# Optimization experiments

Hardware: AMD Instinct MI355X
Metric: run time of the kernel (lower is better)

Reference implementation:

```python
import jax, jax.numpy as jnp
import numpy as np

EPS = 1e-5

def _ln(x, g, b):
    m = jnp.mean(x, -1, keepdims=True)
    v = jnp.mean((x - m) ** 2, -1, keepdims=True)
    return (x - m) * jax.lax.rsqrt(v + EPS) * g + b

def _lstm(x, Wih, Whh, bih, bhh):
    # x: [B, T, D]; torch gate order i, f, g, o; h0 = c0 = 0
    B = x.shape[0]
    H = Whh.shape[1]
    h0 = jnp.zeros((B, H), x.dtype)
    c0 = jnp.zeros((B, H), x.dtype)
    bias = bih + bhh
    def step(carry, xt):
        h, c = carry
        gates = xt @ Wih.T + h @ Whh.T + bias  # [B, 4H]
        i, f, g, o = jnp.split(gates, 4, axis=-1)
        c = jax.nn.sigmoid(f) * c + jax.nn.sigmoid(i) * jnp.tanh(g)
        h = jax.nn.sigmoid(o) * jnp.tanh(c)
        return (h, c), h
    _, hs = jax.lax.scan(step, (h0, c0), jnp.swapaxes(x, 0, 1))
    return jnp.swapaxes(hs, 0, 1)  # [B, T, H]

def setup_inputs() -> dict:
    key = jax.random.key(0)
    ks = jax.random.split(key, 20)
    N, C, F, T = 4, 64, 256, 256
    D, H = 128, 32  # LSTM in/out
    s = 0.05
    inp = {
        "inputs": jax.random.normal(ks[0], (N, C, F, T, 2), jnp.float32),
        "ln1_g": jnp.ones((D,), jnp.float32), "ln1_b": jnp.zeros((D,), jnp.float32),
        "Wih_q": s * jax.random.normal(ks[1], (4 * H, D), jnp.float32),
        "Whh_q": s * jax.random.normal(ks[2], (4 * H, H), jnp.float32),
        "bih_q": s * jax.random.normal(ks[3], (4 * H,), jnp.float32),
        "bhh_q": s * jax.random.normal(ks[4], (4 * H,), jnp.float32),
        "Wih_k": s * jax.random.normal(ks[5], (4 * H, D), jnp.float32),
        "Whh_k": s * jax.random.normal(ks[6], (4 * H, H), jnp.float32),
        "bih_k": s * jax.random.normal(ks[7], (4 * H,), jnp.float32),
        "bhh_k": s * jax.random.normal(ks[8], (4 * H,), jnp.float32),
        "Wih_v": s * jax.random.normal(ks[9], (4 * H, D), jnp.float32),
        "Whh_v": s * jax.random.normal(ks[10], (4 * H, H), jnp.float32),
        "bih_v": s * jax.random.normal(ks[11], (4 * H,), jnp.float32),
        "bhh_v": s * jax.random.normal(ks[12], (4 * H,), jnp.float32),
        "ln2_g": jnp.ones((H,), jnp.float32), "ln2_b": jnp.zeros((H,), jnp.float32),
        "Wr": s * jax.random.normal(ks[13], (C, H // 2), jnp.float32),
        "br": s * jax.random.normal(ks[14], (C,), jnp.float32),
        "Wi": s * jax.random.normal(ks[15], (C, H // 2), jnp.float32),
        "bi": s * jax.random.normal(ks[16], (C,), jnp.float32),
        "ln3_g": jnp.ones((C,), jnp.float32), "ln3_b": jnp.zeros((C,), jnp.float32),
        "prelu_a": jnp.full((1,), 0.25, jnp.float32),
    }
    return inp

def reference(inputs, ln1_g, ln1_b,
              Wih_q, Whh_q, bih_q, bhh_q,
              Wih_k, Whh_k, bih_k, bhh_k,
              Wih_v, Whh_v, bih_v, bhh_v,
              ln2_g, ln2_b, Wr, br, Wi, bi,
              ln3_g, ln3_b, prelu_a):
    N, C, F, T, ri = inputs.shape
    # [N,C,F,T,2] -> [N*F, T, C, 2] -> concat real/imag -> [N*F, T, 2C]
    x4 = jnp.transpose(inputs, (0, 2, 3, 1, 4)).reshape(N * F, T, C, ri)
    x = jnp.concatenate([x4[..., 0], x4[..., 1]], axis=-1)  # [B, T, 128]
    # Self_Attention_T_RICAT (single head)
    xn = _ln(x, ln1_g, ln1_b)
    q = _lstm(xn, Wih_q, Whh_q, bih_q, bhh_q)  # [B, T, 32]
    k = _lstm(xn, Wih_k, Whh_k, bih_k, bhh_k)
    v = _lstm(xn, Wih_v, Whh_v, bih_v, bhh_v)
    energy = jnp.einsum('btf,bsf->bts', q, k) / 4.0  # / 16**0.5
    mask = jnp.tril(jnp.ones((T, T), x.dtype))
    attn = jax.nn.softmax(energy * mask, axis=-1)  # multiplicative mask, as in source
    wv = jnp.einsum('bts,bsf->btf', attn, v)  # [B, T, 32]
    out = _ln(wv, ln2_g, ln2_b)
    # complex-valued linear fusion
    xr, xi = jnp.split(out, 2, axis=-1)  # [B, T, 16] each
    lr_r = xr @ Wr.T + br
    li_i = xi @ Wi.T + bi
    lr_i = xi @ Wr.T + br
    li_r = xr @ Wi.T + bi
    out_real = (lr_r - li_i).reshape(N, F, T, C).transpose(0, 3, 1, 2)  # [N,C,F,T]
    out_imag = (lr_i + li_r).reshape(N, F, T, C).transpose(0, 3, 1, 2)
    outs = jnp.stack([out_real, out_imag], axis=-1)  # [N,C,F,T,2]
    outs_t = jnp.swapaxes(outs, 1, 4)  # [N,2,F,T,C]
    outs = jnp.swapaxes(_ln(outs_t, ln3_g, ln3_b), 1, 4)
    outs = jnp.where(outs >= 0, outs, prelu_a[0] * outs)  # PReLU (eval mode, dropout=identity)
    return outs + inputs
```

## Files before the change

### kernel.cpp

```cpp
#include <hip/hip_runtime.h>
#include <hip/hip_bf16.h>
#include <stddef.h>


typedef __bf16 bf16x8 __attribute__((ext_vector_type(8)));
typedef float f32x4 __attribute__((ext_vector_type(4)));

__device__ __forceinline__ ushort f2bf(float x) {
    uint u = __builtin_bit_cast(uint, x);
    uint r = (u + 0x7fffu + ((u >> 16) & 1u)) >> 16;
    return (ushort)r;
}
__device__ __forceinline__ float bflo2f(uint v) {
    return __builtin_bit_cast(float, v << 16);
}
__device__ __forceinline__ float bfhi2f(uint v) {
    return __builtin_bit_cast(float, v & 0xffff0000u);
}

__device__ __forceinline__ float fsig(float x) {
    return __builtin_amdgcn_rcpf(1.f + __expf(-x));
}
__device__ __forceinline__ float ftanh(float x) {
    return 1.f - 2.f * __builtin_amdgcn_rcpf(__expf(2.f * x) + 1.f);
}
__device__ __forceinline__ float wredsum(float v) {
#pragma unroll
    for (int off = 32; off; off >>= 1) v += __shfl_xor(v, off);
    return v;
}
__device__ __forceinline__ float hredsum(float v) {
#pragma unroll
    for (int off = 16; off; off >>= 1) v += __shfl_xor(v, off);
    return v;
}

__global__ __launch_bounds__(256) void k_prep(const float* __restrict__ in,
                                              const float* __restrict__ g1,
                                              const float* __restrict__ b1,
                                              ushort* __restrict__ xn) {
    __shared__ float xl[32][129];
    const int n = blockIdx.z, f = blockIdx.y, t0 = blockIdx.x * 32;
    const int tid = threadIdx.x;
    const int c = tid >> 2, q = tid & 3;
    const float* src = in + ((size_t)(n * 64 + c) * 256 + f) * 512 + t0 * 2 + q * 16;
#pragma unroll
    for (int e = 0; e < 4; ++e) {
        float4 v4 = *(const float4*)(src + e * 4);
        int dt = q * 8 + e * 2;
        xl[dt][c]          = v4.x;
        xl[dt][c + 64]     = v4.y;
        xl[dt + 1][c]      = v4.z;
        xl[dt + 1][c + 64] = v4.w;
    }
    __syncthreads();
    const int lane = tid & 63, w = tid >> 6;
    const int b = n * 256 + f;
#pragma unroll 1
    for (int r = 0; r < 8; ++r) {
        int dt = w * 8 + r;
        float a = xl[dt][lane], bb = xl[dt][lane + 64];
        float s = wredsum(a + bb);
        float mean = s * 0.0078125f;
        float da = a - mean, db = bb - mean;
        float var = wredsum(da * da + db * db) * 0.0078125f;
        float inv = __builtin_amdgcn_rsqf(var + 1e-5f);
        size_t base = ((size_t)b * 256 + (t0 + dt)) * 128;
        xn[base + lane]      = f2bf(da * inv * g1[lane] + b1[lane]);
        xn[base + lane + 64] = f2bf(db * inv * g1[lane + 64] + b1[lane + 64]);
    }
}

__global__ __launch_bounds__(256) void k_gemm(const ushort* __restrict__ xn,
                                              const float* __restrict__ Wq,
                                              const float* __restrict__ Wk,
                                              const float* __restrict__ Wv,
                                              const float* __restrict__ bihq, const float* __restrict__ bhhq,
                                              const float* __restrict__ bihk, const float* __restrict__ bhhk,
                                              const float* __restrict__ bihv, const float* __restrict__ bhhv,
                                              ushort* __restrict__ gx) {
    __shared__ ushort a_lds[128 * 136];
    __shared__ ushort w_lds[64 * 136];
    const int tid = threadIdx.x;
    const int m0 = blockIdx.x * 128;
    const int yb = blockIdx.y;
    const int l = yb >> 1, n0 = (yb & 1) * 64;
    const float* W   = (l == 0) ? Wq   : (l == 1) ? Wk   : Wv;
    const float* bih = (l == 0) ? bihq : (l == 1) ? bihk : bihv;
    const float* bhh = (l == 0) ? bhhq : (l == 1) ? bhhk : bhhv;

#pragma unroll
    for (int p = 0; p < 8; ++p) {
        int idx = p * 256 + tid;
        int r = idx >> 4, c = idx & 15;
        uint4 v = *(const uint4*)(xn + (size_t)(m0 + r) * 128 + c * 8);
        *(uint4*)&a_lds[r * 136 + c * 8] = v;
    }
#pragma unroll
    for (int p = 0; p < 4; ++p) {
        int idx = p * 256 + tid;
        int r = idx >> 4, c = idx & 15;
        const float* wp = W + (size_t)(n0 + r) * 128 + c * 8;
        float4 wa = *(const float4*)wp;
        float4 wb = *(const float4*)(wp + 4);
        union { ushort u[8]; uint4 v; } pk;
        pk.u[0] = f2bf(wa.x); pk.u[1] = f2bf(wa.y); pk.u[2] = f2bf(wa.z); pk.u[3] = f2bf(wa.w);
        pk.u[4] = f2bf(wb.x); pk.u[5] = f2bf(wb.y); pk.u[6] = f2bf(wb.z); pk.u[7] = f2bf(wb.w);
        *(uint4*)&w_lds[r * 136 + c * 8] = pk.v;
    }
    __syncthreads();

    const int w = tid >> 6, lane = tid & 63;
    const int wr = w >> 1, wc = w & 1;
    const int row16 = lane & 15, koct = lane >> 4;

    f32x4 acc[4][2];
#pragma unroll
    for (int mi = 0; mi < 4; ++mi)
#pragma unroll
        for (int ni = 0; ni < 2; ++ni) acc[mi][ni] = (f32x4){0.f, 0.f, 0.f, 0.f};

#pragma unroll
    for (int ki = 0; ki < 4; ++ki) {
        bf16x8 af[4], bfr[2];
#pragma unroll
        for (int mi = 0; mi < 4; ++mi)
            af[mi] = *(const bf16x8*)&a_lds[(wr * 64 + mi * 16 + row16) * 136 + ki * 32 + koct * 8];
#pragma unroll
        for (int ni = 0; ni < 2; ++ni)
            bfr[ni] = *(const bf16x8*)&w_lds[(wc * 32 + ni * 16 + row16) * 136 + ki * 32 + koct * 8];
#pragma unroll
        for (int mi = 0; mi < 4; ++mi)
#pragma unroll
            for (int ni = 0; ni < 2; ++ni)
                acc[mi][ni] = __builtin_amdgcn_mfma_f32_16x16x32_bf16(af[mi], bfr[ni], acc[mi][ni], 0, 0, 0);
    }

    float bs[2];
#pragma unroll
    for (int ni = 0; ni < 2; ++ni) {
        int ncol = n0 + wc * 32 + ni * 16 + row16;
        bs[ni] = bih[ncol] + bhh[ncol];
    }
#pragma unroll
    for (int mi = 0; mi < 4; ++mi)
#pragma unroll
        for (int ni = 0; ni < 2; ++ni) {
            int ncol = n0 + wc * 32 + ni * 16 + row16;
#pragma unroll
            for (int q = 0; q < 4; ++q) {
                size_t m = (size_t)m0 + wr * 64 + mi * 16 + koct * 4 + q;
                gx[m * 384 + l * 128 + ncol] = f2bf(acc[mi][ni][q] + bs[ni]);
            }
        }
}

__global__ __launch_bounds__(256) void k_lstm(const ushort* __restrict__ gx,
                                              const float* __restrict__ Whq,
                                              const float* __restrict__ Whk,
                                              const float* __restrict__ Whv,
                                              ushort* __restrict__ qkv) {
    __shared__ float hbuf[4][32];
    __shared__ float gbuf[4][128];
    const int tid = threadIdx.x, w = tid >> 6, lane = tid & 63;
    const int sid = blockIdx.x * 4 + w;
    const int l = sid >> 10, b = sid & 1023;
    const float* Wh = (l == 0) ? Whq : (l == 1) ? Whk : Whv;
    float w0[32], w1[32];
    {
        const float4* r0 = (const float4*)(Wh + (size_t)(2 * lane) * 32);
        const float4* r1 = (const float4*)(Wh + (size_t)(2 * lane + 1) * 32);
#pragma unroll
        for (int e = 0; e < 8; ++e) {
            float4 a = r0[e];
            w0[4 * e] = a.x; w0[4 * e + 1] = a.y; w0[4 * e + 2] = a.z; w0[4 * e + 3] = a.w;
            float4 c4 = r1[e];
            w1[4 * e] = c4.x; w1[4 * e + 1] = c4.y; w1[4 * e + 2] = c4.z; w1[4 * e + 3] = c4.w;
        }
    }
    if (lane < 32) hbuf[w][lane] = 0.f;
    float c = 0.f;
    const ushort* gp = gx + (size_t)b * 98304 + l * 128 + 2 * lane;
    ushort* outp = qkv + (size_t)sid * 8192;
    uint gc  = *(const uint*)gp;
    uint g1v = *(const uint*)(gp + 384);
    for (int t = 0; t < 256; ++t) {
        uint g2v = 0;
        if (t + 2 < 256) g2v = *(const uint*)(gp + (size_t)(t + 2) * 384);
        float p0 = 0.f, p1 = 0.f, q0 = 0.f, q1 = 0.f;
#pragma unroll
        for (int jj = 0; jj < 8; ++jj) {
            float4 h4 = *(const float4*)&hbuf[w][jj * 4];
            if (jj & 1) {
                p1 += w0[4 * jj] * h4.x; p1 += w0[4 * jj + 1] * h4.y;
                p1 += w0[4 * jj + 2] * h4.z; p1 += w0[4 * jj + 3] * h4.w;
                q1 += w1[4 * jj] * h4.x; q1 += w1[4 * jj + 1] * h4.y;
                q1 += w1[4 * jj + 2] * h4.z; q1 += w1[4 * jj + 3] * h4.w;
            } else {
                p0 += w0[4 * jj] * h4.x; p0 += w0[4 * jj + 1] * h4.y;
                p0 += w0[4 * jj + 2] * h4.z; p0 += w0[4 * jj + 3] * h4.w;
                q0 += w1[4 * jj] * h4.x; q0 += w1[4 * jj + 1] * h4.y;
                q0 += w1[4 * jj + 2] * h4.z; q0 += w1[4 * jj + 3] * h4.w;
            }
        }
        float g0 = bflo2f(gc) + p0 + p1;
        float g1 = bfhi2f(gc) + q0 + q1;
        *(float2*)&gbuf[w][2 * lane] = make_float2(g0, g1);
        if (lane < 32) {
            float gi = gbuf[w][lane];
            float gf = gbuf[w][lane + 32];
            float gg = gbuf[w][lane + 64];
            float go = gbuf[w][lane + 96];
            c = fsig(gf) * c + fsig(gi) * ftanh(gg);
            float hN = fsig(go) * ftanh(c);
            hbuf[w][lane] = hN;
            outp[(size_t)t * 32 + lane] = f2bf(hN);
        }
        gc = g1v; g1v = g2v;
    }
}

__global__ __launch_bounds__(256) void k_attn(const ushort* __restrict__ qkvb,
                                              float* __restrict__ wvout) {
    __shared__ ushort k_sw[256 * 32];
    __shared__ ushort vt_sw[32 * 256];
    __shared__ ushort p_sw[4][16 * 256];
    const int tid = threadIdx.x, w = tid >> 6, lane = tid & 63;
    const int b = blockIdx.x;
    const ushort* qb = qkvb + (size_t)b * 8192;
    const ushort* kb = qkvb + 8388608 + (size_t)b * 8192;
    const ushort* vb = qkvb + 16777216 + (size_t)b * 8192;
#pragma unroll
    for (int p = 0; p < 4; ++p) {
        int idx = p * 256 + tid;
        int s = idx >> 2, cc = idx & 3;
        uint4 kv = *(const uint4*)(kb + s * 32 + cc * 8);
        int cK = cc ^ ((s >> 1) & 3);
        *(uint4*)&k_sw[s * 32 + cK * 8] = kv;
        uint4 vv = *(const uint4*)(vb + s * 32 + cc * 8);
        union { uint4 v; ushort u[8]; } un; un.v = vv;
#pragma unroll
        for (int e = 0; e < 8; ++e) {
            int row = cc * 8 + e;
            vt_sw[row * 256 + (((s >> 3) ^ (row & 7)) << 3) + (s & 7)] = un.u[e];
        }
    }
    __syncthreads();
    const int r16 = lane & 15, koct = lane >> 4;
    ushort* pw = p_sw[w];
    bf16x8 qf[4];
#pragma unroll
    for (int i = 0; i < 4; ++i) {
        int t = (w * 4 + i) * 16 + r16;
        qf[i] = *(const bf16x8*)(qb + t * 32 + koct * 8);
    }
#pragma unroll 1
    for (int i = 0; i < 4; ++i) {
        const int tb = (w * 4 + i) * 16;
        f32x4 acc[16];
#pragma unroll
        for (int st = 0; st < 16; ++st) acc[st] = (f32x4){0.f, 0.f, 0.f, 0.f};
#pragma unroll
        for (int st = 0; st < 16; ++st) {
            int s = st * 16 + r16;
            int cK = koct ^ ((s >> 1) & 3);
            bf16x8 kf = *(const bf16x8*)&k_sw[s * 32 + cK * 8];
            acc[st] = __builtin_amdgcn_mfma_f32_16x16x32_bf16(qf[i], kf, acc[st], 0, 0, 0);
        }
        float mx[4] = {-1e30f, -1e30f, -1e30f, -1e30f};
#pragma unroll
        for (int st = 0; st < 16; ++st) {
            int s = st * 16 + r16;
#pragma unroll
            for (int q = 0; q < 4; ++q) {
                int t = tb + koct * 4 + q;
                float v = (s <= t) ? acc[st][q] * 0.25f : 0.f;
                acc[st][q] = v;
                mx[q] = fmaxf(mx[q], v);
            }
        }
#pragma unroll
        for (int off = 1; off < 16; off <<= 1)
#pragma unroll
            for (int q = 0; q < 4; ++q) mx[q] = fmaxf(mx[q], __shfl_xor(mx[q], off));
        float sm[4] = {0.f, 0.f, 0.f, 0.f};
#pragma unroll
        for (int st = 0; st < 16; ++st)
#pragma unroll
            for (int q = 0; q < 4; ++q) {
                float p = __expf(acc[st][q] - mx[q]);
                acc[st][q] = p; sm[q] += p;
            }
#pragma unroll
        for (int off = 1; off < 16; off <<= 1)
#pragma unroll
            for (int q = 0; q < 4; ++q) sm[q] += __shfl_xor(sm[q], off);
        float rs[4];
#pragma unroll
        for (int q = 0; q < 4; ++q) rs[q] = __builtin_amdgcn_rcpf(sm[q]);
#pragma unroll
        for (int st = 0; st < 16; ++st) {
            int schunk = st * 2 + (r16 >> 3), sl = r16 & 7;
#pragma unroll
            for (int q = 0; q < 4; ++q) {
                int tl = koct * 4 + q;
                pw[tl * 256 + ((schunk ^ (tl & 7)) << 3) + sl] = f2bf(acc[st][q] * rs[q]);
            }
        }
        __asm__ volatile("s_waitcnt lgkmcnt(0)" ::: "memory");
        f32x4 oa[2];
        oa[0] = (f32x4){0.f, 0.f, 0.f, 0.f};
        oa[1] = (f32x4){0.f, 0.f, 0.f, 0.f};
#pragma unroll
        for (int ks = 0; ks < 8; ++ks) {
            int kc = ks * 4 + koct;
            bf16x8 pa = *(const bf16x8*)&pw[r16 * 256 + ((kc ^ (r16 & 7)) << 3)];
#pragma unroll
            for (int n = 0; n < 2; ++n) {
                int row = n * 16 + r16;
                bf16x8 vf = *(const bf16x8*)&vt_sw[row * 256 + ((kc ^ (row & 7)) << 3)];
                oa[n] = __builtin_amdgcn_mfma_f32_16x16x32_bf16(pa, vf, oa[n], 0, 0, 0);
            }
        }
#pragma unroll
        for (int n = 0; n < 2; ++n)
#pragma unroll
            for (int q = 0; q < 4; ++q)
                wvout[((size_t)b * 256 + tb + koct * 4 + q) * 32 + n * 16 + r16] = oa[n][q];
    }
}

__global__ __launch_bounds__(256) void k_post(const float* __restrict__ wv,
                                              const float* __restrict__ in,
                                              const float* __restrict__ g2,
                                              const float* __restrict__ b2,
                                              const float* __restrict__ Wr,
                                              const float* __restrict__ br,
                                              const float* __restrict__ Wi,
                                              const float* __restrict__ bi,
                                              const float* __restrict__ g3,
                                              const float* __restrict__ b3,
                                              const float* __restrict__ pa,
                                              float* __restrict__ outp) {
    __shared__ float xv[32][33];
    __shared__ float wr_l[64][17], wi_l[64][17];
    __shared__ float out_s[64][65];
    const int tid = threadIdx.x;
    const int n = blockIdx.z, f = blockIdx.y, t0 = blockIdx.x * 32;
    const int b = n * 256 + f;
    for (int idx = tid; idx < 1024; idx += 256) {
        int dt = idx >> 5, j = idx & 31;
        xv[dt][j] = wv[((size_t)b * 256 + t0 + dt) * 32 + j];
        int cc = idx >> 4, jjj = idx & 15;
        wr_l[cc][jjj] = Wr[idx];
        wi_l[cc][jjj] = Wi[idx];
    }
    __syncthreads();
    const int lane = tid & 63, w = tid >> 6;
#pragma unroll 1
    for (int r = 0; r < 4; ++r) {
        int dt = w * 8 + r * 2 + (lane >> 5);
        int j = lane & 31;
        float v = xv[dt][j];
        float mean = hredsum(v) * 0.03125f;
        float d = v - mean;
        float var = hredsum(d * d) * 0.03125f;
        float inv = __builtin_amdgcn_rsqf(var + 1e-5f);
        xv[dt][j] = d * inv * g2[j] + b2[j];
    }
    __syncthreads();
    const int c = lane;
    const float g3c = g3[c], b3c = b3[c];
    const float bd = br[c] - bi[c], bsum = br[c] + bi[c];
    const float alpha = pa[0];
#pragma unroll 1
    for (int r = 0; r < 8; ++r) {
        int dt = w * 8 + r;
        float re = 0.f, im = 0.f;
#pragma unroll
        for (int j = 0; j < 16; ++j) {
            float xr = xv[dt][j], xi2 = xv[dt][16 + j];
            float wrv = wr_l[c][j], wiv = wi_l[c][j];
            re += xr * wrv; re -= xi2 * wiv;
            im += xi2 * wrv; im += xr * wiv;
        }
        re += bd; im += bsum;
        float mR = wredsum(re) * 0.015625f;
        float dR = re - mR;
        float vR = wredsum(dR * dR) * 0.015625f;
        float nR = dR * __builtin_amdgcn_rsqf(vR + 1e-5f) * g3c + b3c;
        nR = (nR >= 0.f) ? nR : alpha * nR;
        float mI = wredsum(im) * 0.015625f;
        float dI = im - mI;
        float vI = wredsum(dI * dI) * 0.015625f;
        float nI = dI * __builtin_amdgcn_rsqf(vI + 1e-5f) * g3c + b3c;
        nI = (nI >= 0.f) ? nI : alpha * nI;
        out_s[c][dt * 2]     = nR;
        out_s[c][dt * 2 + 1] = nI;
    }
    __syncthreads();
    const int cc = tid >> 2, q = tid & 3;
    size_t base = ((size_t)(n * 64 + cc) * 256 + f) * 512 + t0 * 2 + q * 16;
#pragma unroll
    for (int e = 0; e < 4; ++e) {
        float4 iv = *(const float4*)(in + base + e * 4);
        int k0 = q * 16 + e * 4;
        float4 ov;
        ov.x = out_s[cc][k0]     + iv.x;
        ov.y = out_s[cc][k0 + 1] + iv.y;
        ov.z = out_s[cc][k0 + 2] + iv.z;
        ov.w = out_s[cc][k0 + 3] + iv.w;
        *(float4*)(outp + base + e * 4) = ov;
    }
}

extern "C" void kernel_launch(void* const* d_in, const int* in_sizes, int n_in,
                              void* d_out, int out_size, void* d_ws, size_t ws_size,
                              hipStream_t stream) {
    const float* in   = (const float*)d_in[0];
    const float* g1   = (const float*)d_in[1];
    const float* b1   = (const float*)d_in[2];
    const float* Wq   = (const float*)d_in[3];
    const float* Whq  = (const float*)d_in[4];
    const float* bihq = (const float*)d_in[5];
    const float* bhhq = (const float*)d_in[6];
    const float* Wk   = (const float*)d_in[7];
    const float* Whk  = (const float*)d_in[8];
    const float* bihk = (const float*)d_in[9];
    const float* bhhk = (const float*)d_in[10];
    const float* Wv   = (const float*)d_in[11];
    const float* Whv  = (const float*)d_in[12];
    const float* bihv = (const float*)d_in[13];
    const float* bhhv = (const float*)d_in[14];
    const float* g2   = (const float*)d_in[15];
    const float* b2   = (const float*)d_in[16];
    const float* Wr   = (const float*)d_in[17];
    const float* br   = (const float*)d_in[18];
    const float* Wi   = (const float*)d_in[19];
    const float* bi   = (const float*)d_in[20];
    const float* g3   = (const float*)d_in[21];
    const float* b3   = (const float*)d_in[22];
    const float* pa   = (const float*)d_in[23];
    float* outp = (float*)d_out;

    ushort* gxb  = (ushort*)d_ws;
    ushort* xnb  = (ushort*)((char*)d_ws + 201326592);
    ushort* qkvb = (ushort*)((char*)d_ws + 268435456);
    float*  wvb  = (float*)((char*)d_ws + 318767104);

    k_prep<<<dim3(8, 256, 4), dim3(256), 0, stream>>>(in, g1, b1, xnb);
    k_gemm<<<dim3(2048, 6), dim3(256), 0, stream>>>(xnb, Wq, Wk, Wv,
                                                    bihq, bhhq, bihk, bhhk, bihv, bhhv, gxb);
    k_lstm<<<dim3(768), dim3(256), 0, stream>>>(gxb, Whq, Whk, Whv, qkvb);
    k_attn<<<dim3(1024), dim3(256), 0, stream>>>(qkvb, wvb);
    k_post<<<dim3(8, 256, 4), dim3(256), 0, stream>>>(wvb, in, g2, b2,
                                                      Wr, br, Wi, bi, g3, b3, pa, outp);
}
```

Measured before the change: 547.9 us.

## Use fp16 dot2 for LSTM recurrence and redistribute gates via shuffles

Converts the recurrent LSTM weights and hidden state to fp16 and computes the h·Whh product with packed fdot2 instructions. It also permutes the gate layout written by the input-projection kernel so each lane gets paired gates, and exchanges them with a cross-half-wave shuffle instead of a shared-memory gate buffer. All 64 lanes now do the cell update redundantly, removing the idle half-wave and one LDS round trip per timestep. The cost is lower precision in the hidden state and recurrent weights, which accumulates over 256 steps.

```diff
diff --git a/kernel.cpp b/kernel.cpp
--- a/kernel.cpp
+++ b/kernel.cpp
@@ -5,6 +5,8 @@
 
 typedef __bf16 bf16x8 __attribute__((ext_vector_type(8)));
 typedef float f32x4 __attribute__((ext_vector_type(4)));
+typedef _Float16 f16x2 __attribute__((ext_vector_type(2)));
+typedef _Float16 f16x8 __attribute__((ext_vector_type(8)));
 
 __device__ __forceinline__ ushort f2bf(float x) {
     uint u = __builtin_bit_cast(uint, x);
@@ -23,6 +25,13 @@
 }
 __device__ __forceinline__ float ftanh(float x) {
     return 1.f - 2.f * __builtin_amdgcn_rcpf(__expf(2.f * x) + 1.f);
+}
+__device__ __forceinline__ float fdot2(f16x2 a, f16x2 b, float c) {
+#if __has_builtin(__builtin_amdgcn_fdot2)
+    return __builtin_amdgcn_fdot2(a, b, c, false);
+#else
+    return c + (float)a.x * (float)b.x + (float)a.y * (float)b.y;
+#endif
 }
 __device__ __forceinline__ float wredsum(float v) {
 #pragma unroll
@@ -147,10 +156,11 @@
 #pragma unroll
         for (int ni = 0; ni < 2; ++ni) {
             int ncol = n0 + wc * 32 + ni * 16 + row16;
+            int pos = (ncol & 64) | ((ncol >> 5) & 1) | (2 * (ncol & 31));
 #pragma unroll
             for (int q = 0; q < 4; ++q) {
                 size_t m = (size_t)m0 + wr * 64 + mi * 16 + koct * 4 + q;
-                gx[m * 384 + l * 128 + ncol] = f2bf(acc[mi][ni][q] + bs[ni]);
+                gx[m * 384 + l * 128 + pos] = f2bf(acc[mi][ni][q] + bs[ni]);
             }
         }
 }
@@ -160,63 +170,56 @@
                                               const float* __restrict__ Whk,
                                               const float* __restrict__ Whv,
                                               ushort* __restrict__ qkv) {
-    __shared__ float hbuf[4][32];
-    __shared__ float gbuf[4][128];
+    __shared__ _Float16 hbuf[4][64];
     const int tid = threadIdx.x, w = tid >> 6, lane = tid & 63;
+    const int j = lane & 31, hl = lane >> 5;
     const int sid = blockIdx.x * 4 + w;
     const int l = sid >> 10, b = sid & 1023;
     const float* Wh = (l == 0) ? Whq : (l == 1) ? Whk : Whv;
-    float w0[32], w1[32];
+    const int rowA = hl * 64 + j;
+    const int rowB = rowA + 32;
+    f16x2 wA[16], wB[16];
     {
-        const float4* r0 = (const float4*)(Wh + (size_t)(2 * lane) * 32);
-        const float4* r1 = (const float4*)(Wh + (size_t)(2 * lane + 1) * 32);
-#pragma unroll
-        for (int e = 0; e < 8; ++e) {
-            float4 a = r0[e];
-            w0[4 * e] = a.x; w0[4 * e + 1] = a.y; w0[4 * e + 2] = a.z; w0[4 * e + 3] = a.w;
-            float4 c4 = r1[e];
-            w1[4 * e] = c4.x; w1[4 * e + 1] = c4.y; w1[4 * e + 2] = c4.z; w1[4 * e + 3] = c4.w;
-        }
-    }
-    if (lane < 32) hbuf[w][lane] = 0.f;
+        const float* pA = Wh + (size_t)rowA * 32;
+        const float* pB = Wh + (size_t)rowB * 32;
+#pragma unroll
+        for (int e = 0; e < 16; ++e) {
+            wA[e] = f16x2{(_Float16)pA[2 * e], (_Float16)pA[2 * e + 1]};
+            wB[e] = f16x2{(_Float16)pB[2 * e], (_Float16)pB[2 * e + 1]};
+        }
+    }
+    hbuf[w][lane] = (_Float16)0.f;
     float c = 0.f;
-    const ushort* gp = gx + (size_t)b * 98304 + l * 128 + 2 * lane;
+    const ushort* gp = gx + (size_t)b * 98304 + l * 128 + hl * 64 + 2 * j;
     ushort* outp = qkv + (size_t)sid * 8192;
-    uint gc  = *(const uint*)gp;
-    uint g1v = *(const uint*)(gp + 384);
+    uint gc = *(const uint*)gp;
+    uint gn = *(const uint*)(gp + 384);
     for (int t = 0; t < 256; ++t) {
         uint g2v = 0;
         if (t + 2 < 256) g2v = *(const uint*)(gp + (size_t)(t + 2) * 384);
-        float p0 = 0.f, p1 = 0.f, q0 = 0.f, q1 = 0.f;
-#pragma unroll
-        for (int jj = 0; jj < 8; ++jj) {
-            float4 h4 = *(const float4*)&hbuf[w][jj * 4];
-            if (jj & 1) {
-                p1 += w0[4 * jj] * h4.x; p1 += w0[4 * jj + 1] * h4.y;
-                p1 += w0[4 * jj + 2] * h4.z; p1 += w0[4 * jj + 3] * h4.w;
-                q1 += w1[4 * jj] * h4.x; q1 += w1[4 * jj + 1] * h4.y;
-                q1 += w1[4 * jj + 2] * h4.z; q1 += w1[4 * jj + 3] * h4.w;
-            } else {
-                p0 += w0[4 * jj] * h4.x; p0 += w0[4 * jj + 1] * h4.y;
-                p0 += w0[4 * jj + 2] * h4.z; p0 += w0[4 * jj + 3] * h4.w;
-                q0 += w1[4 * jj] * h4.x; q0 += w1[4 * jj + 1] * h4.y;
-                q0 += w1[4 * jj + 2] * h4.z; q0 += w1[4 * jj + 3] * h4.w;
-            }
-        }
-        float g0 = bflo2f(gc) + p0 + p1;
-        float g1 = bfhi2f(gc) + q0 + q1;
-        *(float2*)&gbuf[w][2 * lane] = make_float2(g0, g1);
-        if (lane < 32) {
-            float gi = gbuf[w][lane];
-            float gf = gbuf[w][lane + 32];
-            float gg = gbuf[w][lane + 64];
-            float go = gbuf[w][lane + 96];
-            c = fsig(gf) * c + fsig(gi) * ftanh(gg);
-            float hN = fsig(go) * ftanh(c);
-            hbuf[w][lane] = hN;
-            outp[(size_t)t * 32 + lane] = f2bf(hN);
-        }
-        gc = g1v; g1v = g2v;
+        union { f16x8 v[4]; f16x2 d[16]; } hh;
+        const f16x8* hp = (const f16x8*)&hbuf[w][hl * 32];
+#pragma unroll
+        for (int e = 0; e < 4; ++e) hh.v[e] = hp[e];
+        float a0 = 0.f, a1 = 0.f;
+#pragma unroll
+        for (int e = 0; e < 16; ++e) {
+            a0 = fdot2(hh.d[e], wA[e], a0);
+            a1 = fdot2(hh.d[e], wB[e], a1);
+        }
+        float g0 = bflo2f(gc) + a0;
+        float g1 = bfhi2f(gc) + a1;
+        float xg0 = __shfl_xor(g0, 32);
+        float xg1 = __shfl_xor(g1, 32);
+        float gi = hl ? xg0 : g0;
+        float gf = hl ? xg1 : g1;
+        float gg = hl ? g0 : xg0;
+        float go = hl ? g1 : xg1;
+        c = fsig(gf) * c + fsig(gi) * ftanh(gg);
+        float hN = fsig(go) * ftanh(c);
+        hbuf[w][hl * 32 + j] = (_Float16)hN;
+        if (hl == 0) outp[(size_t)t * 32 + j] = f2bf(hN);
+        gc = gn; gn = g2v;
     }
 }
 
```

Measured after the change: 555.6 us. About the same (+1.4%).
